# Kernel optimization log

Measured on AMD Instinct MI355X. Metric: run time of the kernel, lower is better.

The kernel has to match this reference:

```python
import jax, jax.numpy as jnp
import numpy as np

EPS = 1e-4

def _mp_normalize(x):
    # EDM2-style normalize: divide by (eps + RMS-scaled L2 norm) along last dim -> unit RMS
    n = jnp.linalg.norm(x, axis=-1, keepdims=True)
    n = EPS + n * (1.0 / np.sqrt(x.shape[-1]))
    return x / n

def _mp_linear(x, w):
    # magnitude-preserving linear: row-normalized weight scaled by 1/sqrt(fan_in), no bias
    fan_in = w.shape[-1]
    w_hat = _mp_normalize(w) * (1.0 / np.sqrt(fan_in))
    return x @ w_hat.T

def setup_inputs() -> dict:
    key = jax.random.key(0)
    k1, k2, k3 = jax.random.split(key, 3)
    B, T, D = 2, 2048, 1024
    x = jax.random.normal(k1, (B, T, D), dtype=jnp.float32)
    w_qkv = jax.random.normal(k2, (3 * D, D), dtype=jnp.float32)
    w_out = jax.random.normal(k3, (D, D), dtype=jnp.float32)
    return {"x": x, "w_qkv": w_qkv, "w_out": w_out}

def reference(x, w_qkv, w_out):
    B, T, D = x.shape
    H = 16
    hd = D // H
    scale = 1.0 / np.sqrt(hd)

    qkv = _mp_linear(x, w_qkv)                      # (B, T, 3D)
    q, k, v = jnp.split(qkv, 3, axis=-1)            # each (B, T, D)

    def to_heads(t):
        return t.reshape(B, T, H, hd).transpose(0, 2, 1, 3)  # (B, H, T, hd)

    q, k, v = to_heads(q), to_heads(k), to_heads(v)
    q = _mp_normalize(q)
    k = _mp_normalize(k)

    scores = jnp.einsum("bhqd,bhkd->bhqk", q, k) * scale
    attn = jax.nn.softmax(scores, axis=-1)
    out = jnp.einsum("bhqk,bhkd->bhqd", attn, v)    # (B, H, T, hd)
    out = out.transpose(0, 2, 1, 3).reshape(B, T, D)
    return _mp_linear(out, w_out)
```

## Files before the change

### kernel.cpp

```cpp
#include <hip/hip_runtime.h>

#define BATCH  2
#define SEQ    2048
#define DMODEL 1024
#define NHEAD  16
#define HDIM   64
#define NROWS  (BATCH * SEQ)
#define QKVC   (3 * DMODEL)

typedef float f32x4 __attribute__((ext_vector_type(4)));
typedef float f32x16 __attribute__((ext_vector_type(16)));
typedef short s16x8 __attribute__((ext_vector_type(8)));
typedef short s16x4 __attribute__((ext_vector_type(4)));
typedef unsigned int u32x4 __attribute__((ext_vector_type(4)));

__device__ __forceinline__ unsigned short f2bf(float f) {
  unsigned int u = __float_as_uint(f);
  u = (u + 0x7FFFu + ((u >> 16) & 1u)) >> 16;
  return (unsigned short)u;
}
__device__ __forceinline__ float bf2f(unsigned short s) {
  return __uint_as_float(((unsigned int)s) << 16);
}
__device__ __forceinline__ unsigned pkbf(float a, float b) {
  unsigned r;
  asm("v_cvt_pk_bf16_f32 %0, %1, %2" : "=v"(r) : "v"(a), "v"(b));
  return r;
}
__device__ __forceinline__ void swp(unsigned &a, unsigned &b) {
  asm volatile("v_permlane32_swap_b32 %0, %1" : "+v"(a), "+v"(b));
}

__global__ __launch_bounds__(256) void k_wnorm(const float* __restrict__ Wq_src,
                                               const float* __restrict__ Wo_src,
                                               unsigned short* __restrict__ Wq,
                                               unsigned short* __restrict__ Wo) {
  const int row = blockIdx.x, tid = threadIdx.x;
  const float* src = (row < QKVC) ? (Wq_src + (size_t)row * DMODEL)
                                  : (Wo_src + (size_t)(row - QKVC) * DMODEL);
  unsigned short* dst = (row < QKVC) ? (Wq + (size_t)row * DMODEL)
                                     : (Wo + (size_t)(row - QKVC) * DMODEL);
  float4 v = ((const float4*)src)[tid];
  float ss = v.x * v.x + v.y * v.y + v.z * v.z + v.w * v.w;
#pragma unroll
  for (int m = 1; m < 64; m <<= 1) ss += __shfl_xor(ss, m);
  __shared__ float part[4];
  if ((tid & 63) == 0) part[tid >> 6] = ss;
  __syncthreads();
  const float tot = part[0] + part[1] + part[2] + part[3];
  const float scale = 0.03125f / (1e-4f + sqrtf(tot) * 0.03125f);
  unsigned short* op = dst + tid * 4;
  op[0] = f2bf(v.x * scale); op[1] = f2bf(v.y * scale);
  op[2] = f2bf(v.z * scale); op[3] = f2bf(v.w * scale);
}

__global__ __launch_bounds__(256) void k_cast(const float* __restrict__ X,
                                              unsigned short* __restrict__ Xb) {
  const int i = blockIdx.x * 256 + threadIdx.x;
  const float4 v = ((const float4*)X)[i];
  ushort4 o = { f2bf(v.x), f2bf(v.y), f2bf(v.z), f2bf(v.w) };
  ((ushort4*)Xb)[i] = o;
}

#define LDP 88
template <int WRITE_BF16>
__global__ __launch_bounds__(256, 3) void k_gemm_bt(const unsigned short* __restrict__ A,
                                                    const unsigned short* __restrict__ Bm,
                                                    void* __restrict__ Cv,
                                                    int M, int N, int K) {
  __shared__ unsigned short As[128 * LDP];
  __shared__ unsigned short Bs[128 * LDP];
  const int tid = threadIdx.x;
  const int nbn = N >> 7;
  const int bm = (blockIdx.x / nbn) << 7;
  const int bn = (blockIdx.x % nbn) << 7;
  const int wave = tid >> 6, lane = tid & 63;
  const int wr = (wave >> 1) << 6, wc = (wave & 1) << 6;
  const int l16 = lane & 15, lg = lane >> 4;

  f32x4 acc[4][4];
#pragma unroll
  for (int m = 0; m < 4; ++m)
#pragma unroll
    for (int n = 0; n < 4; ++n) acc[m][n] = (f32x4){0.f, 0.f, 0.f, 0.f};

  s16x8 ra[4], rb[4];
#pragma unroll
  for (int it = 0; it < 4; ++it) {
    const int c = it * 256 + tid;
    const int r = c >> 3, col = (c & 7) << 3;
    ra[it] = *(const s16x8*)(A + (size_t)(bm + r) * K + col);
    rb[it] = *(const s16x8*)(Bm + (size_t)(bn + r) * K + col);
  }

  for (int k0 = 0; k0 < K; k0 += 64) {
    __syncthreads();
#pragma unroll
    for (int it = 0; it < 4; ++it) {
      const int c = it * 256 + tid;
      const int r = c >> 3, col = (c & 7) << 3;
      *(s16x8*)(As + r * LDP + col) = ra[it];
      *(s16x8*)(Bs + r * LDP + col) = rb[it];
    }
    __syncthreads();
    if (k0 + 64 < K) {
#pragma unroll
      for (int it = 0; it < 4; ++it) {
        const int c = it * 256 + tid;
        const int r = c >> 3, col = (c & 7) << 3;
        ra[it] = *(const s16x8*)(A + (size_t)(bm + r) * K + k0 + 64 + col);
        rb[it] = *(const s16x8*)(Bm + (size_t)(bn + r) * K + k0 + 64 + col);
      }
    }
#pragma unroll
    for (int ks = 0; ks < 2; ++ks) {
      s16x8 af[4], bq[4];
#pragma unroll
      for (int m = 0; m < 4; ++m)
        af[m] = *(const s16x8*)(As + (wr + m * 16 + l16) * LDP + ks * 32 + lg * 8);
#pragma unroll
      for (int n = 0; n < 4; ++n)
        bq[n] = *(const s16x8*)(Bs + (wc + n * 16 + l16) * LDP + ks * 32 + lg * 8);
#pragma unroll
      for (int m = 0; m < 4; ++m)
#pragma unroll
        for (int n = 0; n < 4; ++n)
          acc[m][n] = __builtin_amdgcn_mfma_f32_16x16x32_bf16(af[m], bq[n], acc[m][n], 0, 0, 0);
    }
  }
  if (WRITE_BF16) {
    unsigned short* C = (unsigned short*)Cv;
#pragma unroll
    for (int m = 0; m < 4; ++m)
#pragma unroll
      for (int n = 0; n < 4; ++n)
#pragma unroll
        for (int r = 0; r < 4; ++r)
          C[(size_t)(bm + wr + m * 16 + lg * 4 + r) * N + (bn + wc + n * 16 + l16)] =
              f2bf(acc[m][n][r]);
  } else {
    float* C = (float*)Cv;
#pragma unroll
    for (int m = 0; m < 4; ++m)
#pragma unroll
      for (int n = 0; n < 4; ++n)
#pragma unroll
        for (int r = 0; r < 4; ++r)
          C[(size_t)(bm + wr + m * 16 + lg * 4 + r) * N + (bn + wc + n * 16 + l16)] =
              acc[m][n][r];
  }
}

__global__ __launch_bounds__(256) void k_qknorm(unsigned short* __restrict__ qkv) {
  const int row = blockIdx.x, tid = threadIdx.x;
  const int hv = tid >> 3, g = tid & 7;
  const int base = (hv < 16) ? (hv * HDIM) : (DMODEL + (hv - 16) * HDIM);
  unsigned short* p = qkv + (size_t)row * QKVC + base + g * 8;
  s16x8 v = *(const s16x8*)p;
  float f[8];
  float ss = 0.f;
#pragma unroll
  for (int j = 0; j < 8; ++j) { f[j] = bf2f((unsigned short)v[j]); ss += f[j] * f[j]; }
  ss += __shfl_xor(ss, 1); ss += __shfl_xor(ss, 2); ss += __shfl_xor(ss, 4);
  float scale = 1.f / (1e-4f + sqrtf(ss) * 0.125f);
  if (hv < 16) scale *= 0.125f;
  s16x8 o;
#pragma unroll
  for (int j = 0; j < 8; ++j) o[j] = (short)f2bf(f[j] * scale);
  *(s16x8*)p = o;
}

__global__ __launch_bounds__(256) void k_vtrans(const unsigned short* __restrict__ qkv,
                                                unsigned short* __restrict__ Vt) {
  const int tt = blockIdx.x & 31, bh = blockIdx.x >> 5;
  const int b = bh >> 4, h = bh & 15;
  const int t0 = tt * 64;
  __shared__ unsigned short tile[64][80];
  const int tid = threadIdx.x;
#pragma unroll
  for (int half = 0; half < 2; ++half) {
    const int tl = half * 32 + (tid >> 3), part = tid & 7;
    s16x8 v = *(const s16x8*)(qkv + (size_t)(b * SEQ + t0 + tl) * QKVC + 2 * DMODEL +
                              h * HDIM + part * 8);
    *(s16x8*)(&tile[tl][part * 8]) = v;
  }
  __syncthreads();
#pragma unroll
  for (int half = 0; half < 2; ++half) {
    const int d = half * 32 + (tid >> 3), tp = tid & 7;
    s16x8 o;
#pragma unroll
    for (int j = 0; j < 8; ++j) o[j] = (short)tile[tp * 8 + j][d];
    *(s16x8*)(Vt + (size_t)(bh * HDIM + d) * SEQ + t0 + tp * 8) = o;
  }
}

__global__ __launch_bounds__(512) void k_attn(const unsigned short* __restrict__ qkv,
                                              const unsigned short* __restrict__ Vt,
                                              unsigned short* __restrict__ O) {
  const int bid = blockIdx.x;
  const int logical = ((bid & 7) << 6) + (bid >> 3);
  const int bh = logical >> 4, qt = logical & 15;
  const int b = bh >> 4, h = bh & 15;
  const int tid = threadIdx.x;
  const int wave = tid >> 6, lane = tid & 63;
  const int l31 = lane & 31, hi = lane >> 5;
  const int qw = wave & 3, half = wave >> 2;
  const int q0 = qt * 128 + qw * 32;

  __shared__ s16x8 smem[2048];
  __shared__ float LL[4][64];

  s16x8* ksh = smem + half * 512;
  s16x8* vsh = smem + 1024 + half * 512;

  const unsigned short* qp =
      qkv + (size_t)(b * SEQ + q0 + l31) * QKVC + h * HDIM + hi * 8;
  const s16x8 qf0 = *(const s16x8*)(qp);
  const s16x8 qf1 = *(const s16x8*)(qp + 16);
  const s16x8 qf2 = *(const s16x8*)(qp + 32);
  const s16x8 qf3 = *(const s16x8*)(qp + 48);

  const int t8 = tid & 255;
  const int srow = t8 >> 3, chunk = t8 & 7;
  const unsigned short* ksrc =
      qkv + (size_t)(b * SEQ + half * 1024 + srow) * QKVC + DMODEL + h * HDIM + chunk * 8;
  const unsigned short* vsrc =
      Vt + (size_t)(bh * HDIM + srow) * SEQ + half * 1024 + chunk * 8;
  const int wsl = srow * 8 + (chunk ^ (srow & 7));
  const int wsh = wsl + 256;

  f32x16 acc0 = {0,0,0,0,0,0,0,0,0,0,0,0,0,0,0,0};
  f32x16 acc1 = {0,0,0,0,0,0,0,0,0,0,0,0,0,0,0,0};
  float l = 0.f;

  for (int kt = 0; kt < 1024; kt += 64) {
    const s16x8 rk0 = *(const s16x8*)(ksrc + (size_t)kt * QKVC);
    const s16x8 rk1 = *(const s16x8*)(ksrc + (size_t)(kt + 32) * QKVC);
    const s16x8 rv0 = *(const s16x8*)(vsrc + kt);
    const s16x8 rv1 = *(const s16x8*)(vsrc + (size_t)32 * SEQ + kt);
    __syncthreads();
    ksh[wsl] = rk0; ksh[wsh] = rk1;
    vsh[wsl] = rv0; vsh[wsh] = rv1;
    __syncthreads();
#pragma unroll
    for (int kh = 0; kh < 2; ++kh) {
      const int key = kh * 32 + l31;
      const int kb = key * 8, kx = key & 7;
      f32x16 st = {0,0,0,0,0,0,0,0,0,0,0,0,0,0,0,0};
      st = __builtin_amdgcn_mfma_f32_32x32x16_bf16(ksh[kb + ((0 + hi) ^ kx)], qf0, st, 0, 0, 0);
      st = __builtin_amdgcn_mfma_f32_32x32x16_bf16(ksh[kb + ((2 + hi) ^ kx)], qf1, st, 0, 0, 0);
      st = __builtin_amdgcn_mfma_f32_32x32x16_bf16(ksh[kb + ((4 + hi) ^ kx)], qf2, st, 0, 0, 0);
      st = __builtin_amdgcn_mfma_f32_32x32x16_bf16(ksh[kb + ((6 + hi) ^ kx)], qf3, st, 0, 0, 0);

#pragma unroll
      for (int r = 0; r < 16; ++r) st[r] = __expf(st[r] - 8.f);

      float s0 = (st[0] + st[1]) + (st[2] + st[3]);
      float s1 = (st[4] + st[5]) + (st[6] + st[7]);
      float s2 = (st[8] + st[9]) + (st[10] + st[11]);
      float s3 = (st[12] + st[13]) + (st[14] + st[15]);
      l += (s0 + s1) + (s2 + s3);

      unsigned P0 = pkbf(st[0], st[1]),   P1 = pkbf(st[2], st[3]);
      unsigned P2 = pkbf(st[4], st[5]),   P3 = pkbf(st[6], st[7]);
      unsigned P4 = pkbf(st[8], st[9]),   P5 = pkbf(st[10], st[11]);
      unsigned P6 = pkbf(st[12], st[13]), P7 = pkbf(st[14], st[15]);
      swp(P0, P2);
      swp(P1, P3);
      swp(P4, P6);
      swp(P5, P7);
      u32x4 w0; w0[0] = P0; w0[1] = P1; w0[2] = P2; w0[3] = P3;
      u32x4 w1; w1[0] = P4; w1[1] = P5; w1[2] = P6; w1[3] = P7;
      const s16x8 pf0 = __builtin_bit_cast(s16x8, w0);
      const s16x8 pf1 = __builtin_bit_cast(s16x8, w1);

      const int vb0 = l31 * 8,        vx0 = l31 & 7;
      const int vb1 = (l31 + 32) * 8, vx1 = vx0;
      acc0 = __builtin_amdgcn_mfma_f32_32x32x16_bf16(vsh[vb0 + ((kh * 4 + 0 + hi) ^ vx0)], pf0, acc0, 0, 0, 0);
      acc0 = __builtin_amdgcn_mfma_f32_32x32x16_bf16(vsh[vb0 + ((kh * 4 + 2 + hi) ^ vx0)], pf1, acc0, 0, 0, 0);
      acc1 = __builtin_amdgcn_mfma_f32_32x32x16_bf16(vsh[vb1 + ((kh * 4 + 0 + hi) ^ vx1)], pf0, acc1, 0, 0, 0);
      acc1 = __builtin_amdgcn_mfma_f32_32x32x16_bf16(vsh[vb1 + ((kh * 4 + 2 + hi) ^ vx1)], pf1, acc1, 0, 0, 0);
    }
  }

  l += __shfl_xor(l, 32);

  __syncthreads();
  float* OO = (float*)smem;
  if (half) {
    float* o_ = OO + qw * 2048;
#pragma unroll
    for (int r = 0; r < 16; ++r) {
      o_[r * 64 + lane] = acc0[r];
      o_[(16 + r) * 64 + lane] = acc1[r];
    }
    LL[qw][lane] = l;
  }
  __syncthreads();
  if (!half) {
    const float inv = 1.f / (l + LL[qw][lane]);
    const float* o_ = OO + qw * 2048;
    unsigned short* ob = O + (size_t)(b * SEQ + q0 + l31) * DMODEL + h * HDIM;
#pragma unroll
    for (int g = 0; g < 4; ++g) {
      float e00 = (acc0[4 * g]     + o_[(4 * g) * 64 + lane])     * inv;
      float e01 = (acc0[4 * g + 1] + o_[(4 * g + 1) * 64 + lane]) * inv;
      float e02 = (acc0[4 * g + 2] + o_[(4 * g + 2) * 64 + lane]) * inv;
      float e03 = (acc0[4 * g + 3] + o_[(4 * g + 3) * 64 + lane]) * inv;
      float e10 = (acc1[4 * g]     + o_[(16 + 4 * g) * 64 + lane])     * inv;
      float e11 = (acc1[4 * g + 1] + o_[(16 + 4 * g + 1) * 64 + lane]) * inv;
      float e12 = (acc1[4 * g + 2] + o_[(16 + 4 * g + 2) * 64 + lane]) * inv;
      float e13 = (acc1[4 * g + 3] + o_[(16 + 4 * g + 3) * 64 + lane]) * inv;
      s16x4 o0 = { (short)f2bf(e00), (short)f2bf(e01), (short)f2bf(e02), (short)f2bf(e03) };
      s16x4 o1 = { (short)f2bf(e10), (short)f2bf(e11), (short)f2bf(e12), (short)f2bf(e13) };
      *(s16x4*)(ob + g * 8 + hi * 4) = o0;
      *(s16x4*)(ob + 32 + g * 8 + hi * 4) = o1;
    }
  }
}

extern "C" void kernel_launch(void* const* d_in, const int* in_sizes, int n_in,
                              void* d_out, int out_size, void* d_ws, size_t ws_size,
                              hipStream_t stream) {
  const float* x    = (const float*)d_in[0];
  const float* wqkv = (const float*)d_in[1];
  const float* wout = (const float*)d_in[2];
  char* ws = (char*)d_ws;
  unsigned short* Wq  = (unsigned short*)(ws);
  unsigned short* Wo  = (unsigned short*)(ws + 6291456);
  unsigned short* Xb  = (unsigned short*)(ws + 8388608);
  unsigned short* QKV = (unsigned short*)(ws + 16777216);
  unsigned short* Vt  = (unsigned short*)(ws + 41943040);
  (void)in_sizes; (void)n_in; (void)out_size; (void)ws_size;

  k_wnorm<<<QKVC + DMODEL, 256, 0, stream>>>(wqkv, wout, Wq, Wo);
  k_cast<<<(NROWS * DMODEL) / 1024, 256, 0, stream>>>(x, Xb);
  k_gemm_bt<1><<<(NROWS / 128) * (QKVC / 128), 256, 0, stream>>>(
      Xb, Wq, (void*)QKV, NROWS, QKVC, DMODEL);
  k_qknorm<<<NROWS, 256, 0, stream>>>(QKV);
  k_vtrans<<<BATCH * NHEAD * (SEQ / 64), 256, 0, stream>>>(QKV, Vt);
  k_attn<<<BATCH * NHEAD * 16, 512, 0, stream>>>(QKV, Vt, Xb);
  k_gemm_bt<0><<<(NROWS / 128) * (DMODEL / 128), 256, 0, stream>>>(
      Xb, Wo, d_out, NROWS, DMODEL, DMODEL);
}
```

Baseline: 122.7 us.

## Fuse per-head Q/K normalization and V transpose into QKV GEMM epilogue

The QKV projection GEMM now computes per-head RMS normalization of Q and K in its epilogue, using register values and lane shuffles across the 64-column wave tile. V tiles are written directly in transposed layout to the Vt buffer. This removes the separate k_qknorm and k_vtrans launches along with their extra global read/write passes over the QKV buffer. The cost is a heavier GEMM epilogue with shuffles and strided 8-byte Vt stores. Because V is no longer written to the QKV buffer, correctness depends on the attention kernel reading V only from Vt.

```diff
diff --git a/kernel.cpp b/kernel.cpp
--- a/kernel.cpp
+++ b/kernel.cpp
@@ -63,11 +63,11 @@
 }
 
 #define LDP 88
-template <int WRITE_BF16>
-__global__ __launch_bounds__(256, 3) void k_gemm_bt(const unsigned short* __restrict__ A,
-                                                    const unsigned short* __restrict__ Bm,
-                                                    void* __restrict__ Cv,
-                                                    int M, int N, int K) {
+__global__ __launch_bounds__(256, 3) void k_gemm_qkv(const unsigned short* __restrict__ A,
+                                                     const unsigned short* __restrict__ Bm,
+                                                     unsigned short* __restrict__ C,
+                                                     unsigned short* __restrict__ Vt) {
+  const int M = NROWS, N = QKVC, K = DMODEL;
   __shared__ unsigned short As[128 * LDP];
   __shared__ unsigned short Bs[128 * LDP];
   const int tid = threadIdx.x;
@@ -128,71 +128,115 @@
           acc[m][n] = __builtin_amdgcn_mfma_f32_16x16x32_bf16(af[m], bq[n], acc[m][n], 0, 0, 0);
     }
   }
-  if (WRITE_BF16) {
-    unsigned short* C = (unsigned short*)Cv;
+
+  const int colbase = bn + wc;
+  if (colbase < 2 * DMODEL) {
+    const float qmul = (colbase < DMODEL) ? 0.125f : 1.0f;
 #pragma unroll
     for (int m = 0; m < 4; ++m)
 #pragma unroll
+      for (int r = 0; r < 4; ++r) {
+        float ss = 0.f;
+#pragma unroll
+        for (int n = 0; n < 4; ++n) ss += acc[m][n][r] * acc[m][n][r];
+        ss += __shfl_xor(ss, 1); ss += __shfl_xor(ss, 2);
+        ss += __shfl_xor(ss, 4); ss += __shfl_xor(ss, 8);
+        const float scale = qmul / (1e-4f + sqrtf(ss) * 0.125f);
+#pragma unroll
+        for (int n = 0; n < 4; ++n)
+          C[(size_t)(bm + wr + m * 16 + lg * 4 + r) * N + (colbase + n * 16 + l16)] =
+              f2bf(acc[m][n][r] * scale);
+      }
+  } else {
+    const int hv = (colbase - 2 * DMODEL) >> 6;
+    const int token0 = bm + wr;
+    const int b_ = token0 >> 11;
+    const int bh = b_ * NHEAD + hv;
+    const int t0 = (token0 & (SEQ - 1)) + lg * 4;
+#pragma unroll
+    for (int m = 0; m < 4; ++m)
+#pragma unroll
+      for (int n = 0; n < 4; ++n) {
+        const int d = n * 16 + l16;
+        s16x4 ov = { (short)f2bf(acc[m][n][0]), (short)f2bf(acc[m][n][1]),
+                     (short)f2bf(acc[m][n][2]), (short)f2bf(acc[m][n][3]) };
+        *(s16x4*)(Vt + (size_t)(bh * HDIM + d) * SEQ + t0 + m * 16) = ov;
+      }
+  }
+}
+
+__global__ __launch_bounds__(256, 3) void k_gemm_out(const unsigned short* __restrict__ A,
+                                                     const unsigned short* __restrict__ Bm,
+                                                     float* __restrict__ C,
+                                                     int M, int N, int K) {
+  __shared__ unsigned short As[128 * LDP];
+  __shared__ unsigned short Bs[128 * LDP];
+  const int tid = threadIdx.x;
+  const int nbn = N >> 7;
+  const int bm = (blockIdx.x / nbn) << 7;
+  const int bn = (blockIdx.x % nbn) << 7;
+  const int wave = tid >> 6, lane = tid & 63;
+  const int wr = (wave >> 1) << 6, wc = (wave & 1) << 6;
+  const int l16 = lane & 15, lg = lane >> 4;
+
+  f32x4 acc[4][4];
+#pragma unroll
+  for (int m = 0; m < 4; ++m)
+#pragma unroll
+    for (int n = 0; n < 4; ++n) acc[m][n] = (f32x4){0.f, 0.f, 0.f, 0.f};
+
+  s16x8 ra[4], rb[4];
+#pragma unroll
+  for (int it = 0; it < 4; ++it) {
+    const int c = it * 256 + tid;
+    const int r = c >> 3, col = (c & 7) << 3;
+    ra[it] = *(const s16x8*)(A + (size_t)(bm + r) * K + col);
+    rb[it] = *(const s16x8*)(Bm + (size_t)(bn + r) * K + col);
+  }
+
+  for (int k0 = 0; k0 < K; k0 += 64) {
+    __syncthreads();
+#pragma unroll
+    for (int it = 0; it < 4; ++it) {
+      const int c = it * 256 + tid;
+      const int r = c >> 3, col = (c & 7) << 3;
+      *(s16x8*)(As + r * LDP + col) = ra[it];
+      *(s16x8*)(Bs + r * LDP + col) = rb[it];
+    }
+    __syncthreads();
+    if (k0 + 64 < K) {
+#pragma unroll
+      for (int it = 0; it < 4; ++it) {
+        const int c = it * 256 + tid;
+        const int r = c >> 3, col = (c & 7) << 3;
+        ra[it] = *(const s16x8*)(A + (size_t)(bm + r) * K + k0 + 64 + col);
+        rb[it] = *(const s16x8*)(Bm + (size_t)(bn + r) * K + k0 + 64 + col);
+      }
+    }
+#pragma unroll
+    for (int ks = 0; ks < 2; ++ks) {
+      s16x8 af[4], bq[4];
+#pragma unroll
+      for (int m = 0; m < 4; ++m)
+        af[m] = *(const s16x8*)(As + (wr + m * 16 + l16) * LDP + ks * 32 + lg * 8);
+#pragma unroll
       for (int n = 0; n < 4; ++n)
-#pragma unroll
-        for (int r = 0; r < 4; ++r)
-          C[(size_t)(bm + wr + m * 16 + lg * 4 + r) * N + (bn + wc + n * 16 + l16)] =
-              f2bf(acc[m][n][r]);
-  } else {
-    float* C = (float*)Cv;
-#pragma unroll
-    for (int m = 0; m < 4; ++m)
-#pragma unroll
-      for (int n = 0; n < 4; ++n)
-#pragma unroll
-        for (int r = 0; r < 4; ++r)
-          C[(size_t)(bm + wr + m * 16 + lg * 4 + r) * N + (bn + wc + n * 16 + l16)] =
-              acc[m][n][r];
-  }
-}
-
-__global__ __launch_bounds__(256) void k_qknorm(unsigned short* __restrict__ qkv) {
-  const int row = blockIdx.x, tid = threadIdx.x;
-  const int hv = tid >> 3, g = tid & 7;
-  const int base = (hv < 16) ? (hv * HDIM) : (DMODEL + (hv - 16) * HDIM);
-  unsigned short* p = qkv + (size_t)row * QKVC + base + g * 8;
-  s16x8 v = *(const s16x8*)p;
-  float f[8];
-  float ss = 0.f;
-#pragma unroll
-  for (int j = 0; j < 8; ++j) { f[j] = bf2f((unsigned short)v[j]); ss += f[j] * f[j]; }
-  ss += __shfl_xor(ss, 1); ss += __shfl_xor(ss, 2); ss += __shfl_xor(ss, 4);
-  float scale = 1.f / (1e-4f + sqrtf(ss) * 0.125f);
-  if (hv < 16) scale *= 0.125f;
-  s16x8 o;
-#pragma unroll
-  for (int j = 0; j < 8; ++j) o[j] = (short)f2bf(f[j] * scale);
-  *(s16x8*)p = o;
-}
-
-__global__ __launch_bounds__(256) void k_vtrans(const unsigned short* __restrict__ qkv,
-                                                unsigned short* __restrict__ Vt) {
-  const int tt = blockIdx.x & 31, bh = blockIdx.x >> 5;
-  const int b = bh >> 4, h = bh & 15;
-  const int t0 = tt * 64;
-  __shared__ unsigned short tile[64][80];
-  const int tid = threadIdx.x;
-#pragma unroll
-  for (int half = 0; half < 2; ++half) {
-    const int tl = half * 32 + (tid >> 3), part = tid & 7;
-    s16x8 v = *(const s16x8*)(qkv + (size_t)(b * SEQ + t0 + tl) * QKVC + 2 * DMODEL +
-                              h * HDIM + part * 8);
-    *(s16x8*)(&tile[tl][part * 8]) = v;
-  }
-  __syncthreads();
-#pragma unroll
-  for (int half = 0; half < 2; ++half) {
-    const int d = half * 32 + (tid >> 3), tp = tid & 7;
-    s16x8 o;
-#pragma unroll
-    for (int j = 0; j < 8; ++j) o[j] = (short)tile[tp * 8 + j][d];
-    *(s16x8*)(Vt + (size_t)(bh * HDIM + d) * SEQ + t0 + tp * 8) = o;
-  }
+        bq[n] = *(const s16x8*)(Bs + (wc + n * 16 + l16) * LDP + ks * 32 + lg * 8);
+#pragma unroll
+      for (int m = 0; m < 4; ++m)
+#pragma unroll
+        for (int n = 0; n < 4; ++n)
+          acc[m][n] = __builtin_amdgcn_mfma_f32_16x16x32_bf16(af[m], bq[n], acc[m][n], 0, 0, 0);
+    }
+  }
+#pragma unroll
+  for (int m = 0; m < 4; ++m)
+#pragma unroll
+    for (int n = 0; n < 4; ++n)
+#pragma unroll
+      for (int r = 0; r < 4; ++r)
+        C[(size_t)(bm + wr + m * 16 + lg * 4 + r) * N + (bn + wc + n * 16 + l16)] =
+            acc[m][n][r];
 }
 
 __global__ __launch_bounds__(512) void k_attn(const unsigned short* __restrict__ qkv,
@@ -336,11 +380,8 @@
 
   k_wnorm<<<QKVC + DMODEL, 256, 0, stream>>>(wqkv, wout, Wq, Wo);
   k_cast<<<(NROWS * DMODEL) / 1024, 256, 0, stream>>>(x, Xb);
-  k_gemm_bt<1><<<(NROWS / 128) * (QKVC / 128), 256, 0, stream>>>(
-      Xb, Wq, (void*)QKV, NROWS, QKVC, DMODEL);
-  k_qknorm<<<NROWS, 256, 0, stream>>>(QKV);
-  k_vtrans<<<BATCH * NHEAD * (SEQ / 64), 256, 0, stream>>>(QKV, Vt);
+  k_gemm_qkv<<<(NROWS / 128) * (QKVC / 128), 256, 0, stream>>>(Xb, Wq, QKV, Vt);
   k_attn<<<BATCH * NHEAD * 16, 512, 0, stream>>>(QKV, Vt, Xb);
-  k_gemm_bt<0><<<(NROWS / 128) * (DMODEL / 128), 256, 0, stream>>>(
-      Xb, Wo, d_out, NROWS, DMODEL, DMODEL);
-}
+  k_gemm_out<<<(NROWS / 128) * (DMODEL / 128), 256, 0, stream>>>(
+      Xb, Wo, (float*)d_out, NROWS, DMODEL, DMODEL);
+}
```

Result: faster. 114.6 us (-6.6%).
